# Kernel tuning notes

Measured on AMD Instinct MI355X. Metric: run time of the kernel, lower is better.

The kernel has to match this reference:

```python
import jax, jax.numpy as jnp
import numpy as np

D_MODEL = 1024
NUM_HEADS = 16
HEAD_DIM = D_MODEL // NUM_HEADS
B, L = 2, 2048


def setup_inputs() -> dict:
    key = jax.random.key(0)
    ks = jax.random.split(key, 9)
    s = 0.02
    return {
        "query": jax.random.normal(ks[0], (B, L, D_MODEL), dtype=jnp.float32),
        "key": jax.random.normal(ks[1], (B, L, D_MODEL), dtype=jnp.float32),
        "value": jax.random.normal(ks[2], (B, L, D_MODEL), dtype=jnp.float32),
        "mask": jax.random.randint(ks[3], (B, L), 0, 2, dtype=jnp.int32),
        "Wq": jax.random.normal(ks[4], (D_MODEL, D_MODEL), dtype=jnp.float32) * s,
        "Wk": jax.random.normal(ks[5], (D_MODEL, D_MODEL), dtype=jnp.float32) * s,
        "Wv": jax.random.normal(ks[6], (D_MODEL, D_MODEL), dtype=jnp.float32) * s,
        "Wo": jax.random.normal(ks[7], (D_MODEL, D_MODEL), dtype=jnp.float32) * s,
        "bo": jnp.zeros((D_MODEL,), dtype=jnp.float32),
    }


def _split_heads(x):
    # (B, L, d_model) -> (B, H, L, head_dim)
    b, l, _ = x.shape
    return x.reshape(b, l, NUM_HEADS, HEAD_DIM).transpose(0, 2, 1, 3)


def reference(query, key, value, mask, Wq, Wk, Wv, Wo, bo):
    # nn.Linear(bias=False): x @ W.T
    q = _split_heads(query @ Wq.T)   # (B, H, L, hd)
    k = _split_heads(key @ Wk.T)
    v = _split_heads(value @ Wv.T)

    scores = jnp.einsum("bhqd,bhkd->bhqk", q, k) / jnp.sqrt(jnp.float32(HEAD_DIM))
    # padding mask over keys: (B, L) -> (B, 1, 1, L); 0 = pad -> -inf
    keep = (mask[:, None, None, :] != 0)
    scores = jnp.where(keep, scores, -jnp.inf)

    attn = jax.nn.softmax(scores, axis=-1)
    # original zeroes NaN rows (fully-masked query rows)
    attn = jnp.where(jnp.isnan(attn), jnp.zeros_like(attn), attn)
    # dropout is identity in eval/reference mode

    ctx = jnp.einsum("bhqk,bhkd->bhqd", attn, v)           # (B, H, L, hd)
    ctx = ctx.transpose(0, 2, 1, 3).reshape(B, L, D_MODEL)  # combine heads
    return ctx @ Wo.T + bo
```

## Files before the change

kernel.cpp:

```cpp
#include <hip/hip_runtime.h>

typedef unsigned short u16;
typedef __bf16 bf16x8 __attribute__((ext_vector_type(8)));
typedef __bf16 bf16x4 __attribute__((ext_vector_type(4)));
typedef float floatx4 __attribute__((ext_vector_type(4)));
typedef u16 u16x4 __attribute__((ext_vector_type(4)));

#define MEG ((size_t)(1u << 20))

__device__ __forceinline__ u16 f2bf(float f) {
  unsigned int u = __float_as_uint(f);
  u += 0x7fffu + ((u >> 16) & 1u);
  return (u16)(u >> 16);
}

__device__ __forceinline__ void load_lds16(const u16* g, u16* l) {
  __builtin_amdgcn_global_load_lds((const __attribute__((address_space(1))) unsigned int*)g,
                                   (__attribute__((address_space(3))) unsigned int*)l,
                                   16, 0, 0);
}

__global__ __launch_bounds__(256) void cvt7(
    const float* __restrict__ s0, const float* __restrict__ s1,
    const float* __restrict__ s2, const float* __restrict__ s3,
    const float* __restrict__ s4, const float* __restrict__ s5,
    const float* __restrict__ s6, u16* __restrict__ dst)
{
  size_t e = ((size_t)blockIdx.x * 256 + threadIdx.x) * 4;
  unsigned m = (unsigned)(e >> 20);
  const float* s; size_t off;
  if (m < 4)       { s = s0; off = e; }
  else if (m < 8)  { s = s1; off = e - 4 * MEG; }
  else if (m < 12) { s = s2; off = e - 8 * MEG; }
  else if (m < 13) { s = s3; off = e - 12 * MEG; }
  else if (m < 14) { s = s4; off = e - 13 * MEG; }
  else if (m < 15) { s = s5; off = e - 14 * MEG; }
  else             { s = s6; off = e - 15 * MEG; }
  float4 f = *reinterpret_cast<const float4*>(s + off);
  u16x4 o;
  o.x = f2bf(f.x); o.y = f2bf(f.y); o.z = f2bf(f.z); o.w = f2bf(f.w);
  *reinterpret_cast<u16x4*>(dst + e) = o;
}

template<int IT, bool OUT_BF16, bool ADD_BIAS>
__global__ __launch_bounds__(256) void gemm_bt(
    const u16* __restrict__ Abase, const u16* __restrict__ Bbase,
    const float* __restrict__ bias, void* __restrict__ Cbase,
    int M, int N, int K, long zA, long zB, long zC)
{
  __shared__ __align__(16) u16 As[IT * 32 * 64];
  __shared__ __align__(16) u16 Bs[128 * 64];
  const int tid = threadIdx.x;
  const int w = tid >> 6, ln = tid & 63;
  const int lm = ln & 15, lq = ln >> 4;
  const int wm = w >> 1, wn = w & 1;
  const long m0 = (long)blockIdx.y * (IT * 32), n0 = (long)blockIdx.x * 128;
  const u16* A = Abase + (size_t)blockIdx.z * (size_t)zA;
  const u16* B = Bbase + (size_t)blockIdx.z * (size_t)zB;

  const int r0 = tid >> 3;
  const int kc = (tid & 7) ^ (r0 & 7);
  const u16* gA = A + (m0 + r0) * (long)K + kc * 8;
  const u16* gB = B + (n0 + r0) * (long)K + kc * 8;
  const long rstep = 32L * K;

  const int sl0 = (lq ^ (lm & 7)) * 8;
  const int sl1 = ((4 + lq) ^ (lm & 7)) * 8;
  const u16* ab0 = &As[(wm * (IT * 16) + lm) * 64 + sl0];
  const u16* ab1 = &As[(wm * (IT * 16) + lm) * 64 + sl1];
  const u16* bb0 = &Bs[(wn * 64 + lm) * 64 + sl0];
  const u16* bb1 = &Bs[(wn * 64 + lm) * 64 + sl1];

  const floatx4 z4 = {0.f, 0.f, 0.f, 0.f};
  floatx4 acc[IT][4];
#pragma unroll
  for (int i = 0; i < IT; ++i)
#pragma unroll
    for (int j = 0; j < 4; ++j) acc[i][j] = z4;

  for (int k0 = 0; k0 < K; k0 += 64) {
#pragma unroll
    for (int t = 0; t < IT; ++t)
      load_lds16(gA + t * rstep, &As[(t * 256 + w * 64) * 8]);
#pragma unroll
    for (int t = 0; t < 4; ++t)
      load_lds16(gB + t * rstep, &Bs[(t * 256 + w * 64) * 8]);
    gA += 64; gB += 64;
    __syncthreads();
    bf16x8 af[IT][2], bfr[4][2];
#pragma unroll
    for (int i = 0; i < IT; ++i) {
      af[i][0] = *reinterpret_cast<const bf16x8*>(ab0 + i * 1024);
      af[i][1] = *reinterpret_cast<const bf16x8*>(ab1 + i * 1024);
    }
#pragma unroll
    for (int j = 0; j < 4; ++j) {
      bfr[j][0] = *reinterpret_cast<const bf16x8*>(bb0 + j * 1024);
      bfr[j][1] = *reinterpret_cast<const bf16x8*>(bb1 + j * 1024);
    }
#pragma unroll
    for (int i = 0; i < IT; ++i)
#pragma unroll
      for (int j = 0; j < 4; ++j) {
        acc[i][j] = __builtin_amdgcn_mfma_f32_16x16x32_bf16(af[i][0], bfr[j][0], acc[i][j], 0, 0, 0);
        acc[i][j] = __builtin_amdgcn_mfma_f32_16x16x32_bf16(af[i][1], bfr[j][1], acc[i][j], 0, 0, 0);
      }
    __syncthreads();
  }

#pragma unroll
  for (int i = 0; i < IT; ++i) {
    long row = m0 + wm * (IT * 16) + i * 16 + lq * 4;
#pragma unroll
    for (int j = 0; j < 4; ++j) {
      long col = n0 + wn * 64 + j * 16 + lm;
#pragma unroll
      for (int r = 0; r < 4; ++r) {
        float v = acc[i][j][r];
        if (ADD_BIAS) v += bias[col];
        size_t idx = (size_t)(row + r) * (size_t)N + (size_t)col;
        if (OUT_BF16) (((u16*)Cbase) + (size_t)blockIdx.z * (size_t)zC)[idx] = f2bf(v);
        else ((float*)Cbase)[idx] = v;
      }
    }
  }
}

__global__ __launch_bounds__(256) void transpose_v(const u16* __restrict__ Vp, u16* __restrict__ Vt)
{
  __shared__ u16 T[64 * 80];
  const int tid = threadIdx.x;
  const int bh = blockIdx.y, b = bh >> 4, h = bh & 15;
  const int l0 = blockIdx.x * 64;
#pragma unroll
  for (int t = 0; t < 2; ++t) {
    int ci = t * 256 + tid;
    int l = ci >> 3, c = ci & 7;
    *reinterpret_cast<uint4*>(&T[l * 80 + c * 8]) =
      *reinterpret_cast<const uint4*>(&Vp[((size_t)(b * 2048 + l0 + l)) * 1024 + h * 64 + c * 8]);
  }
  __syncthreads();
#pragma unroll
  for (int t = 0; t < 2; ++t) {
    int ci = t * 256 + tid;
    int d = ci >> 3, lg = ci & 7;
    u16 tmp[8];
#pragma unroll
    for (int s = 0; s < 8; ++s) tmp[s] = T[(lg * 8 + s) * 80 + d];
    *reinterpret_cast<uint4*>(&Vt[(size_t)bh * 131072 + (size_t)d * 2048 + l0 + lg * 8]) =
      *reinterpret_cast<uint4*>(tmp);
  }
}

__global__ __launch_bounds__(256, 2) void attn_kernel(
    const u16* __restrict__ Qp, const u16* __restrict__ Kp,
    const u16* __restrict__ Vt, const int* __restrict__ mask,
    u16* __restrict__ ctx)
{
  __shared__ __align__(16) u16 Ks[64 * 64];
  __shared__ __align__(16) u16 Vts[64 * 64];
  __shared__ __align__(16) u16 Ps[4 * 32 * 64];
  __shared__ __align__(16) float mball[2048];

  const int tid = threadIdx.x;
  const int w = tid >> 6, ln = tid & 63;
  const int lm = ln & 15, lq = ln >> 4;
  const int bh = blockIdx.y, b = bh >> 4, h = bh & 15;
  const int q0 = blockIdx.x * 128;

  const u16* Qh = Qp + (size_t)b * 2048 * 1024 + h * 64;
  const u16* Kh = Kp + (size_t)b * 2048 * 1024 + h * 64;
  const u16* Vth = Vt + (size_t)bh * 64 * 2048;

  const int* mrowp = mask + b * 2048;
#pragma unroll
  for (int t = 0; t < 8; ++t) {
    int i = t * 256 + tid;
    mball[i] = (mrowp[i] != 0) ? 0.f : -1e30f;
  }

  bf16x8 qf[2][2];
#pragma unroll
  for (int m = 0; m < 2; ++m) {
    int qrow = q0 + w * 32 + m * 16 + lm;
    qf[m][0] = *reinterpret_cast<const bf16x8*>(Qh + (size_t)qrow * 1024 + lq * 8);
    qf[m][1] = *reinterpret_cast<const bf16x8*>(Qh + (size_t)qrow * 1024 + 32 + lq * 8);
  }

  const int sl0 = (lq ^ (lm & 7)) * 8;
  const int sl1 = ((4 + lq) ^ (lm & 7)) * 8;
  const u16* kb0 = &Ks[lm * 64 + sl0];
  const u16* kb1 = &Ks[lm * 64 + sl1];
  const u16* vb0 = &Vts[lm * 64 + sl0];
  const u16* vb1 = &Vts[lm * 64 + sl1];
  u16* Pw = &Ps[w * 2048];
  u16* pwr[4];
#pragma unroll
  for (int n = 0; n < 4; ++n) pwr[n] = &Pw[lm * 64 + (((4 * n + lq) ^ lm) * 4)];
  const u16* prd[4];
#pragma unroll
  for (int t = 0; t < 4; ++t)
    prd[t] = &Pw[lm * 64 + (((8 * (t >> 1) + 2 * lq + (t & 1)) ^ lm) * 4)];
  const float* mbi = mball + lq * 4;

  const int r0 = tid >> 3;
  const int kc = (tid & 7) ^ (r0 & 7);
  const u16* gK0 = Kh + (size_t)r0 * 1024 + kc * 8;
  const u16* gK1 = gK0 + 32 * 1024;
  const u16* gV0 = Vth + (size_t)r0 * 2048 + kc * 8;
  const u16* gV1 = gV0 + 32 * 2048;

  const floatx4 z4 = {0.f, 0.f, 0.f, 0.f};
  floatx4 O[2][4];
#pragma unroll
  for (int m = 0; m < 2; ++m)
#pragma unroll
    for (int j = 0; j < 4; ++j) O[m][j] = z4;
  float psum[2] = {0.f, 0.f};
  const float SCL = 0.18033688011112042f;

  for (int it = 0; it < 32; ++it) {
    load_lds16(gK0, &Ks[(w * 64) * 8]);
    load_lds16(gK1, &Ks[(256 + w * 64) * 8]);
    load_lds16(gV0, &Vts[(w * 64) * 8]);
    load_lds16(gV1, &Vts[(256 + w * 64) * 8]);
    gK0 += 64 * 1024; gK1 += 64 * 1024; gV0 += 64; gV1 += 64;
    __syncthreads();

    bf16x8 kf[4][2], vf[4][2];
#pragma unroll
    for (int n = 0; n < 4; ++n) {
      kf[n][0] = *reinterpret_cast<const bf16x8*>(kb0 + n * 1024);
      kf[n][1] = *reinterpret_cast<const bf16x8*>(kb1 + n * 1024);
    }
#pragma unroll
    for (int j = 0; j < 4; ++j) {
      vf[j][0] = *reinterpret_cast<const bf16x8*>(vb0 + j * 1024);
      vf[j][1] = *reinterpret_cast<const bf16x8*>(vb1 + j * 1024);
    }

#pragma unroll
    for (int m = 0; m < 2; ++m) {
      floatx4 S[4];
#pragma unroll
      for (int n = 0; n < 4; ++n) {
        S[n] = __builtin_amdgcn_mfma_f32_16x16x32_bf16(kf[n][0], qf[m][0], z4, 0, 0, 0);
        S[n] = __builtin_amdgcn_mfma_f32_16x16x32_bf16(kf[n][1], qf[m][1], S[n], 0, 0, 0);
      }

#pragma unroll
      for (int n = 0; n < 4; ++n) {
        float4 m4 = *reinterpret_cast<const float4*>(mbi + n * 16);
        float p0 = __builtin_amdgcn_exp2f(fmaf(S[n][0], SCL, m4.x));
        float p1 = __builtin_amdgcn_exp2f(fmaf(S[n][1], SCL, m4.y));
        float p2 = __builtin_amdgcn_exp2f(fmaf(S[n][2], SCL, m4.z));
        float p3 = __builtin_amdgcn_exp2f(fmaf(S[n][3], SCL, m4.w));
        psum[m] += (p0 + p1) + (p2 + p3);
        unsigned u0 = __float_as_uint(p0) + 0x8000u;
        unsigned u1 = __float_as_uint(p1) + 0x8000u;
        unsigned u2 = __float_as_uint(p2) + 0x8000u;
        unsigned u3 = __float_as_uint(p3) + 0x8000u;
        uint2 pk;
        pk.x = __builtin_amdgcn_perm(u1, u0, 0x07060302u);
        pk.y = __builtin_amdgcn_perm(u3, u2, 0x07060302u);
        *reinterpret_cast<uint2*>(pwr[n] + m * 1024) = pk;
      }

#pragma unroll
      for (int h2 = 0; h2 < 2; ++h2) {
        bf16x4 pa = *reinterpret_cast<const bf16x4*>(prd[2 * h2] + m * 1024);
        bf16x4 pb = *reinterpret_cast<const bf16x4*>(prd[2 * h2 + 1] + m * 1024);
        bf16x8 pf = __builtin_shufflevector(pa, pb, 0, 1, 2, 3, 4, 5, 6, 7);
#pragma unroll
        for (int j = 0; j < 4; ++j)
          O[m][j] = __builtin_amdgcn_mfma_f32_16x16x32_bf16(pf, vf[j][h2], O[m][j], 0, 0, 0);
      }
    }
    mbi += 64;
    __syncthreads();
  }

#pragma unroll
  for (int m = 0; m < 2; ++m) {
    float s = psum[m];
    s += __shfl_xor(s, 16, 64);
    s += __shfl_xor(s, 32, 64);
#pragma unroll
    for (int r = 0; r < 4; ++r) {
      int srcl = (ln & 48) | (lq * 4 + r);
      float inv = 1.0f / __shfl(s, srcl, 64);
      int row = q0 + w * 32 + m * 16 + lq * 4 + r;
      size_t base = ((size_t)b * 2048 + row) * 1024 + h * 64 + lm;
#pragma unroll
      for (int j = 0; j < 4; ++j)
        ctx[base + j * 16] = f2bf(O[m][j][r] * inv);
    }
  }
}

extern "C" void kernel_launch(void* const* d_in, const int* in_sizes, int n_in,
                              void* d_out, int out_size, void* d_ws, size_t ws_size,
                              hipStream_t stream) {
  const float* q  = (const float*)d_in[0];
  const float* k  = (const float*)d_in[1];
  const float* v  = (const float*)d_in[2];
  const int*   mk = (const int*)  d_in[3];
  const float* wq = (const float*)d_in[4];
  const float* wk = (const float*)d_in[5];
  const float* wv = (const float*)d_in[6];
  const float* wo = (const float*)d_in[7];
  const float* bo = (const float*)d_in[8];

  u16* ws16 = (u16*)d_ws;
  u16* Xq  = ws16;
  u16* Wq  = ws16 + 12 * MEG;
  u16* Wo  = ws16 + 15 * MEG;
  u16* Qp  = ws16 + 16 * MEG;
  u16* Kp  = ws16 + 20 * MEG;
  u16* Vp  = ws16 + 24 * MEG;
  u16* Vt  = ws16;
  u16* ctx = ws16 + 4 * MEG;

  cvt7<<<dim3(16384), dim3(256), 0, stream>>>(q, k, v, wq, wk, wv, wo, ws16);

  gemm_bt<4, true, false><<<dim3(8, 32, 3), dim3(256), 0, stream>>>(
      Xq, Wq, nullptr, (void*)Qp, 4096, 1024, 1024,
      (long)(4 * MEG), (long)MEG, (long)(4 * MEG));

  transpose_v<<<dim3(32, 32), dim3(256), 0, stream>>>(Vp, Vt);

  attn_kernel<<<dim3(16, 32), dim3(256), 0, stream>>>(Qp, Kp, Vt, mk, ctx);

  gemm_bt<2, false, true><<<dim3(8, 64, 1), dim3(256), 0, stream>>>(
      ctx, Wo, bo, d_out, 4096, 1024, 1024, 0, 0, 0);
}
```

Measured before the change: 227.2 us.

## Fuse V transpose into projection GEMM epilogue and shrink attention mask LDS

```diff
diff --git a/kernel.cpp b/kernel.cpp
--- a/kernel.cpp
+++ b/kernel.cpp
@@ -42,10 +42,11 @@
   *reinterpret_cast<u16x4*>(dst + e) = o;
 }
 
-template<int IT, bool OUT_BF16, bool ADD_BIAS>
+template<int IT, bool OUT_BF16, bool ADD_BIAS, bool VT>
 __global__ __launch_bounds__(256) void gemm_bt(
     const u16* __restrict__ Abase, const u16* __restrict__ Bbase,
     const float* __restrict__ bias, void* __restrict__ Cbase,
+    u16* __restrict__ VtB,
     int M, int N, int K, long zA, long zB, long zC)
 {
   __shared__ __align__(16) u16 As[IT * 32 * 64];
@@ -108,6 +109,26 @@
     __syncthreads();
   }
 
+  if (VT && blockIdx.z == 2) {
+#pragma unroll
+    for (int i = 0; i < IT; ++i) {
+      long row = m0 + wm * (IT * 16) + i * 16 + lq * 4;
+      int bq = (int)(row >> 11);
+      int l  = (int)(row & 2047);
+#pragma unroll
+      for (int j = 0; j < 4; ++j) {
+        long col = n0 + wn * 64 + j * 16 + lm;
+        int hh = (int)(col >> 6), dd = (int)(col & 63);
+        u16x4 o;
+        o.x = f2bf(acc[i][j][0]); o.y = f2bf(acc[i][j][1]);
+        o.z = f2bf(acc[i][j][2]); o.w = f2bf(acc[i][j][3]);
+        *reinterpret_cast<u16x4*>(&VtB[((size_t)(bq * 16 + hh)) * 131072 +
+                                       (size_t)dd * 2048 + l]) = o;
+      }
+    }
+    return;
+  }
+
 #pragma unroll
   for (int i = 0; i < IT; ++i) {
     long row = m0 + wm * (IT * 16) + i * 16 + lq * 4;
@@ -126,33 +147,7 @@
   }
 }
 
-__global__ __launch_bounds__(256) void transpose_v(const u16* __restrict__ Vp, u16* __restrict__ Vt)
-{
-  __shared__ u16 T[64 * 80];
-  const int tid = threadIdx.x;
-  const int bh = blockIdx.y, b = bh >> 4, h = bh & 15;
-  const int l0 = blockIdx.x * 64;
-#pragma unroll
-  for (int t = 0; t < 2; ++t) {
-    int ci = t * 256 + tid;
-    int l = ci >> 3, c = ci & 7;
-    *reinterpret_cast<uint4*>(&T[l * 80 + c * 8]) =
-      *reinterpret_cast<const uint4*>(&Vp[((size_t)(b * 2048 + l0 + l)) * 1024 + h * 64 + c * 8]);
-  }
-  __syncthreads();
-#pragma unroll
-  for (int t = 0; t < 2; ++t) {
-    int ci = t * 256 + tid;
-    int d = ci >> 3, lg = ci & 7;
-    u16 tmp[8];
-#pragma unroll
-    for (int s = 0; s < 8; ++s) tmp[s] = T[(lg * 8 + s) * 80 + d];
-    *reinterpret_cast<uint4*>(&Vt[(size_t)bh * 131072 + (size_t)d * 2048 + l0 + lg * 8]) =
-      *reinterpret_cast<uint4*>(tmp);
-  }
-}
-
-__global__ __launch_bounds__(256, 2) void attn_kernel(
+__global__ __launch_bounds__(256, 4) void attn_kernel(
     const u16* __restrict__ Qp, const u16* __restrict__ Kp,
     const u16* __restrict__ Vt, const int* __restrict__ mask,
     u16* __restrict__ ctx)
@@ -160,7 +155,7 @@
   __shared__ __align__(16) u16 Ks[64 * 64];
   __shared__ __align__(16) u16 Vts[64 * 64];
   __shared__ __align__(16) u16 Ps[4 * 32 * 64];
-  __shared__ __align__(16) float mball[2048];
+  __shared__ __align__(16) u16 mball[2048];
 
   const int tid = threadIdx.x;
   const int w = tid >> 6, ln = tid & 63;
@@ -176,7 +171,7 @@
 #pragma unroll
   for (int t = 0; t < 8; ++t) {
     int i = t * 256 + tid;
-    mball[i] = (mrowp[i] != 0) ? 0.f : -1e30f;
+    mball[i] = (mrowp[i] != 0) ? (u16)0 : (u16)0xFF80;
   }
 
   bf16x8 qf[2][2];
@@ -201,7 +196,7 @@
 #pragma unroll
   for (int t = 0; t < 4; ++t)
     prd[t] = &Pw[lm * 64 + (((8 * (t >> 1) + 2 * lq + (t & 1)) ^ lm) * 4)];
-  const float* mbi = mball + lq * 4;
+  const u16* mbi = mball + lq * 4;
 
   const int r0 = tid >> 3;
   const int kc = (tid & 7) ^ (r0 & 7);
@@ -238,6 +233,15 @@
       vf[j][0] = *reinterpret_cast<const bf16x8*>(vb0 + j * 1024);
       vf[j][1] = *reinterpret_cast<const bf16x8*>(vb1 + j * 1024);
     }
+    float mb4[4][4];
+#pragma unroll
+    for (int n = 0; n < 4; ++n) {
+      u16x4 mv = *reinterpret_cast<const u16x4*>(mbi + n * 16);
+      mb4[n][0] = __uint_as_float((unsigned)mv.x << 16);
+      mb4[n][1] = __uint_as_float((unsigned)mv.y << 16);
+      mb4[n][2] = __uint_as_float((unsigned)mv.z << 16);
+      mb4[n][3] = __uint_as_float((unsigned)mv.w << 16);
+    }
 
 #pragma unroll
     for (int m = 0; m < 2; ++m) {
@@ -250,11 +254,10 @@
 
 #pragma unroll
       for (int n = 0; n < 4; ++n) {
-        float4 m4 = *reinterpret_cast<const float4*>(mbi + n * 16);
-        float p0 = __builtin_amdgcn_exp2f(fmaf(S[n][0], SCL, m4.x));
-        float p1 = __builtin_amdgcn_exp2f(fmaf(S[n][1], SCL, m4.y));
-        float p2 = __builtin_amdgcn_exp2f(fmaf(S[n][2], SCL, m4.z));
-        float p3 = __builtin_amdgcn_exp2f(fmaf(S[n][3], SCL, m4.w));
+        float p0 = __builtin_amdgcn_exp2f(fmaf(S[n][0], SCL, mb4[n][0]));
+        float p1 = __builtin_amdgcn_exp2f(fmaf(S[n][1], SCL, mb4[n][1]));
+        float p2 = __builtin_amdgcn_exp2f(fmaf(S[n][2], SCL, mb4[n][2]));
+        float p3 = __builtin_amdgcn_exp2f(fmaf(S[n][3], SCL, mb4[n][3]));
         psum[m] += (p0 + p1) + (p2 + p3);
         unsigned u0 = __float_as_uint(p0) + 0x8000u;
         unsigned u1 = __float_as_uint(p1) + 0x8000u;
@@ -317,20 +320,17 @@
   u16* Wo  = ws16 + 15 * MEG;
   u16* Qp  = ws16 + 16 * MEG;
   u16* Kp  = ws16 + 20 * MEG;
-  u16* Vp  = ws16 + 24 * MEG;
-  u16* Vt  = ws16;
+  u16* Vt  = ws16 + 24 * MEG;
   u16* ctx = ws16 + 4 * MEG;
 
   cvt7<<<dim3(16384), dim3(256), 0, stream>>>(q, k, v, wq, wk, wv, wo, ws16);
 
-  gemm_bt<4, true, false><<<dim3(8, 32, 3), dim3(256), 0, stream>>>(
-      Xq, Wq, nullptr, (void*)Qp, 4096, 1024, 1024,
+  gemm_bt<4, true, false, true><<<dim3(8, 32, 3), dim3(256), 0, stream>>>(
+      Xq, Wq, nullptr, (void*)Qp, Vt, 4096, 1024, 1024,
       (long)(4 * MEG), (long)MEG, (long)(4 * MEG));
 
-  transpose_v<<<dim3(32, 32), dim3(256), 0, stream>>>(Vp, Vt);
-
   attn_kernel<<<dim3(16, 32), dim3(256), 0, stream>>>(Qp, Kp, Vt, mk, ctx);
 
-  gemm_bt<2, false, true><<<dim3(8, 64, 1), dim3(256), 0, stream>>>(
-      ctx, Wo, bo, d_out, 4096, 1024, 1024, 0, 0, 0);
-}
+  gemm_bt<2, false, true, false><<<dim3(8, 64, 1), dim3(256), 0, stream>>>(
+      ctx, Wo, bo, d_out, nullptr, 4096, 1024, 1024, 0, 0, 0);
+}
```

Result: no change. 230.8 us (+1.6%).
